# Performance work log

Hardware: AMD Instinct MI355X
Metric: run time of the kernel (lower is better)

The kernel has to match this reference:

```python
import jax, jax.numpy as jnp
import numpy as np

THRESHOLD = 6.2
N_SECTIONS = 9      # n_conv_sections
SEC_LEN = 4         # n_section_length
SEC_H = 9           # n_input_sections + n_section_length - 1
BATCH = 16384


def setup_inputs() -> dict:
    key = jax.random.key(0)
    k1, k2 = jax.random.split(key)
    # input spike-wave tensor [T, C=1, H=41, W=40]
    x = jax.random.uniform(k1, (BATCH, 1, 41, 40), dtype=jnp.float32)
    # per-section conv weights, N(0.8, 0.05) as in snn.Convolution init
    W = 0.8 + 0.05 * jax.random.normal(k2, (N_SECTIONS, 50, 1, 6, 40), dtype=jnp.float32)
    return {"x": x, "W": W}


def _conv(sec, w):
    # sec: [B,1,9,40], w: [50,1,6,40] -> [B,50,4,1]
    return jax.lax.conv_general_dilated(
        sec, w, window_strides=(1, 1), padding='VALID',
        dimension_numbers=('NCHW', 'OIHW', 'NCHW'))


def reference(x, W):
    # slice the 9 overlapping input sections -> [9, B, 1, 9, 40]
    sec = jnp.stack([x[:, :, i * SEC_LEN:i * SEC_LEN + SEC_H, :]
                     for i in range(N_SECTIONS)])
    pots = jax.vmap(_conv)(sec, W)                      # [9, B, 50, 4, 1]
    pots = jnp.max(pots, axis=3, keepdims=True)         # Pooling((4,1)) -> [9, B, 50, 1, 1]
    spks = jnp.where(pots > THRESHOLD, 1.0, 0.0).astype(pots.dtype)
    # concat sections along height (dim=2 of [B,C,H,W])
    pots_cat = jnp.moveaxis(pots[:, :, :, 0, :], 0, 2)  # [B, 50, 9, 1]
    spks_cat = jnp.moveaxis(spks[:, :, :, 0, :], 0, 2)  # [B, 50, 9, 1]
    return pots_cat, spks_cat
```

## Files before the change

### kernel.cpp

```cpp
#include <hip/hip_runtime.h>
#include <cstdint>
#include <cstddef>

#define NBATCH   16384
#define NSEC     9
#define NOC      50
#define NOCP     64
#define KREAL    240
#define KPAD     256
#define XROW     1640
#define SECELEMS 360
#define XS       392
#define OUTHALF  7372800
#define THRESH   6.2f

typedef _Float16 half8  __attribute__((ext_vector_type(8)));
typedef _Float16 half4v __attribute__((ext_vector_type(4)));
typedef float    f32x4  __attribute__((ext_vector_type(4)));

__global__ __launch_bounds__(256)
void wconv_kernel(const float* __restrict__ W, _Float16* __restrict__ wks) {
    int idx = blockIdx.x * 256 + threadIdx.x;
    int k   = idx & 255;
    int ocp = (idx >> 8) & 63;
    int sec = idx >> 14;
    float v = 0.0f;
    if (ocp < NOC && k < KREAL)
        v = W[(size_t)(sec * NOC + ocp) * KREAL + k];
    wks[idx] = (_Float16)v;
}

__global__ __launch_bounds__(256)
void conv_mfma_kernel(const float* __restrict__ x,
                      const _Float16* __restrict__ wks,
                      float* __restrict__ pots_tmp) {
    __shared__ _Float16 xs[64 * XS];

    const int tid  = threadIdx.x;
    const int tile = blockIdx.x;
    const int sec  = blockIdx.y;

    {
        half8 z = {};
        int b  = tid >> 2;
        int ko = SECELEMS + (tid & 3) * 8;
        *(half8*)&xs[b * XS + ko] = z;
    }

    const float* xg = x + (size_t)(tile * 64) * XROW + sec * 160;
    for (int c = tid; c < 64 * 90; c += 256) {
        int b  = c / 90;
        int cc = c - b * 90;
        float4 v = *(const float4*)(xg + (size_t)b * XROW + cc * 4);
        half4v h;
        h.x = (_Float16)v.x; h.y = (_Float16)v.y;
        h.z = (_Float16)v.z; h.w = (_Float16)v.w;
        *(half4v*)&xs[b * XS + cc * 4] = h;
    }
    __syncthreads();

    const int lane = tid & 63;
    const int wave = tid >> 6;
    const int l15  = lane & 15;
    const int quad = lane >> 4;

    f32x4 acc[4][4] = {};

    const _Float16* xrow = xs + (wave * 16 + l15) * XS;
    const _Float16* wrow = wks + (size_t)sec * (NOCP * KPAD) + l15 * KPAD;

    #pragma unroll
    for (int kk = 0; kk < 8; ++kk) {
        const int kb = kk * 32 + quad * 8;
        half8 av[4], bv[4];
        #pragma unroll
        for (int h = 0; h < 4; ++h)
            av[h] = *(const half8*)(xrow + h * 40 + kb);
        #pragma unroll
        for (int n = 0; n < 4; ++n)
            bv[n] = *(const half8*)(wrow + n * 16 * KPAD + kb);
        #pragma unroll
        for (int h = 0; h < 4; ++h)
            #pragma unroll
            for (int n = 0; n < 4; ++n)
                acc[h][n] = __builtin_amdgcn_mfma_f32_16x16x32_f16(
                                av[h], bv[n], acc[h][n], 0, 0, 0);
    }

    const int bbase = tile * 64 + wave * 16 + quad * 4;
    #pragma unroll
    for (int nt = 0; nt < 4; ++nt) {
        int oc = nt * 16 + l15;
        if (oc < NOC) {
            #pragma unroll
            for (int r = 0; r < 4; ++r) {
                float p = acc[0][nt][r];
                p = fmaxf(p, acc[1][nt][r]);
                p = fmaxf(p, acc[2][nt][r]);
                p = fmaxf(p, acc[3][nt][r]);
                pots_tmp[((size_t)sec * NBATCH + bbase + r) * NOC + oc] = p;
            }
        }
    }
}

__global__ __launch_bounds__(256)
void transpose_kernel(const float* __restrict__ pots_tmp,
                      float* __restrict__ out) {
    __shared__ float t[32 * 450];
    const int tid = threadIdx.x;
    const int b0  = blockIdx.x * 32;

    for (int i = tid; i < NSEC * 32 * NOC; i += 256) {
        int sec = i / (32 * NOC);
        int r   = i - sec * (32 * NOC);
        int b   = r / NOC;
        int oc  = r - b * NOC;
        float v = pots_tmp[((size_t)sec * NBATCH + b0 + b) * NOC + oc];
        t[b * 450 + oc * NSEC + sec] = v;
    }
    __syncthreads();

    float* spk = out + OUTHALF;
    for (int i = tid; i < 32 * 450; i += 256) {
        float v = t[i];
        size_t g = (size_t)b0 * 450 + i;
        out[g] = v;
        spk[g] = (v > THRESH) ? 1.0f : 0.0f;
    }
}

__global__ __launch_bounds__(256)
void naive_kernel(const float* __restrict__ x, const float* __restrict__ W,
                  float* __restrict__ out) {
    size_t idx = (size_t)blockIdx.x * 256 + threadIdx.x;
    if (idx >= OUTHALF) return;
    int s  = (int)(idx % NSEC);
    int oc = (int)((idx / NSEC) % NOC);
    int b  = (int)(idx / (NSEC * NOC));
    const float* xb = x + (size_t)b * XROW + s * 160;
    const float* w  = W + (size_t)(s * NOC + oc) * KREAL;
    float best = -1e30f;
    for (int h0 = 0; h0 < 4; ++h0) {
        float acc = 0.0f;
        for (int t = 0; t < KREAL; ++t)
            acc += xb[h0 * 40 + t] * w[t];
        best = fmaxf(best, acc);
    }
    out[idx] = best;
    out[OUTHALF + idx] = (best > THRESH) ? 1.0f : 0.0f;
}

extern "C" void kernel_launch(void* const* d_in, const int* in_sizes, int n_in,
                              void* d_out, int out_size, void* d_ws, size_t ws_size,
                              hipStream_t stream) {
    const float* x = (const float*)d_in[0];
    const float* W = (const float*)d_in[1];
    float* out = (float*)d_out;

    const size_t w_bytes   = (size_t)NSEC * NOCP * KPAD * sizeof(_Float16);
    const size_t pot_bytes = (size_t)NSEC * NBATCH * NOC * sizeof(float);

    if (ws_size < w_bytes + pot_bytes) {
        naive_kernel<<<(OUTHALF + 255) / 256, 256, 0, stream>>>(x, W, out);
        return;
    }

    _Float16* wks     = (_Float16*)d_ws;
    float*    potstmp = (float*)((char*)d_ws + w_bytes);

    wconv_kernel<<<(NSEC * NOCP * KPAD) / 256, 256, 0, stream>>>(W, wks);

    dim3 grid(NBATCH / 64, NSEC);
    conv_mfma_kernel<<<grid, 256, 0, stream>>>(x, wks, potstmp);

    transpose_kernel<<<NBATCH / 32, 256, 0, stream>>>(potstmp, out);
}
```

Measured before the change: 239.0 us.

## Fuse conv and transpose into one kernel processing all sections per batch tile

Merges the per-section MFMA conv kernel and the separate transpose kernel into one kernel. Each block loads a 16-sample batch tile once, loops over all 9 sections with each wave owning 16 output channels, and transposes the results through LDS before writing pots and spikes. This drops the pots_tmp round trip through global memory and one launch, and it reads x once instead of re-reading the overlapping section slices. The cost is a smaller MFMA tile per wave, more LDS per block (about 53 KB), and weights reloaded from global for each section.

Measured after the change: 236.7 us. No clear change (-1.0%).

```diff
diff --git a/kernel.cpp b/kernel.cpp
--- a/kernel.cpp
+++ b/kernel.cpp
@@ -9,8 +9,8 @@
 #define KREAL    240
 #define KPAD     256
 #define XROW     1640
-#define SECELEMS 360
-#define XS       392
+#define XS2      1672
+#define TB       16
 #define OUTHALF  7372800
 #define THRESH   6.2f
 
@@ -30,103 +30,85 @@
     wks[idx] = (_Float16)v;
 }
 
-__global__ __launch_bounds__(256)
-void conv_mfma_kernel(const float* __restrict__ x,
-                      const _Float16* __restrict__ wks,
-                      float* __restrict__ pots_tmp) {
-    __shared__ _Float16 xs[64 * XS];
+__global__ __launch_bounds__(256, 3)
+void fused_kernel(const float* __restrict__ x,
+                  const _Float16* __restrict__ wks,
+                  float* __restrict__ out) {
+    __shared__ __align__(16) _Float16 xs[TB * XS2];
 
-    const int tid  = threadIdx.x;
-    const int tile = blockIdx.x;
-    const int sec  = blockIdx.y;
+    const int tid = threadIdx.x;
+    const size_t b0 = (size_t)blockIdx.x * TB;
 
-    {
+    if (tid < 32) {
         half8 z = {};
-        int b  = tid >> 2;
-        int ko = SECELEMS + (tid & 3) * 8;
-        *(half8*)&xs[b * XS + ko] = z;
+        int b = tid >> 1, off = XROW + (tid & 1) * 8;
+        *(half8*)&xs[b * XS2 + off] = z;
     }
 
-    const float* xg = x + (size_t)(tile * 64) * XROW + sec * 160;
-    for (int c = tid; c < 64 * 90; c += 256) {
-        int b  = c / 90;
-        int cc = c - b * 90;
+    const float* xg = x + b0 * XROW;
+    for (int c = tid; c < TB * 410; c += 256) {
+        int b = c / 410, cc = c - b * 410;
         float4 v = *(const float4*)(xg + (size_t)b * XROW + cc * 4);
         half4v h;
         h.x = (_Float16)v.x; h.y = (_Float16)v.y;
         h.z = (_Float16)v.z; h.w = (_Float16)v.w;
-        *(half4v*)&xs[b * XS + cc * 4] = h;
+        *(half4v*)&xs[b * XS2 + cc * 4] = h;
     }
     __syncthreads();
 
     const int lane = tid & 63;
-    const int wave = tid >> 6;
+    const int w    = tid >> 6;
     const int l15  = lane & 15;
     const int quad = lane >> 4;
 
-    f32x4 acc[4][4] = {};
+    const _Float16* xrow = xs + l15 * XS2 + quad * 8;
+    const _Float16* wrow = wks + (size_t)(w * 16 + l15) * KPAD + quad * 8;
 
-    const _Float16* xrow = xs + (wave * 16 + l15) * XS;
-    const _Float16* wrow = wks + (size_t)sec * (NOCP * KPAD) + l15 * KPAD;
+    f32x4 res[NSEC];
 
-    #pragma unroll
-    for (int kk = 0; kk < 8; ++kk) {
-        const int kb = kk * 32 + quad * 8;
-        half8 av[4], bv[4];
+    for (int s = 0; s < NSEC; ++s) {
+        const _Float16* wsec = wrow + (size_t)s * (NOCP * KPAD);
+        half8 bv[8];
         #pragma unroll
-        for (int h = 0; h < 4; ++h)
-            av[h] = *(const half8*)(xrow + h * 40 + kb);
+        for (int kk = 0; kk < 8; ++kk)
+            bv[kk] = *(const half8*)(wsec + kk * 32);
+
+        f32x4 acc[4] = {f32x4{}, f32x4{}, f32x4{}, f32x4{}};
+        const _Float16* xsec = xrow + s * 160;
         #pragma unroll
-        for (int n = 0; n < 4; ++n)
-            bv[n] = *(const half8*)(wrow + n * 16 * KPAD + kb);
+        for (int kk = 0; kk < 8; ++kk) {
+            #pragma unroll
+            for (int h = 0; h < 4; ++h) {
+                half8 av = *(const half8*)(xsec + h * 40 + kk * 32);
+                acc[h] = __builtin_amdgcn_mfma_f32_16x16x32_f16(
+                             av, bv[kk], acc[h], 0, 0, 0);
+            }
+        }
+        f32x4 r;
         #pragma unroll
-        for (int h = 0; h < 4; ++h)
-            #pragma unroll
-            for (int n = 0; n < 4; ++n)
-                acc[h][n] = __builtin_amdgcn_mfma_f32_16x16x32_f16(
-                                av[h], bv[n], acc[h][n], 0, 0, 0);
+        for (int j = 0; j < 4; ++j)
+            r[j] = fmaxf(fmaxf(acc[0][j], acc[1][j]),
+                         fmaxf(acc[2][j], acc[3][j]));
+        res[s] = r;
     }
 
-    const int bbase = tile * 64 + wave * 16 + quad * 4;
-    #pragma unroll
-    for (int nt = 0; nt < 4; ++nt) {
-        int oc = nt * 16 + l15;
-        if (oc < NOC) {
+    __syncthreads();
+    float* t = (float*)xs;
+    const int oc = w * 16 + l15;
+    if (oc < NOC) {
+        #pragma unroll
+        for (int s = 0; s < NSEC; ++s)
             #pragma unroll
-            for (int r = 0; r < 4; ++r) {
-                float p = acc[0][nt][r];
-                p = fmaxf(p, acc[1][nt][r]);
-                p = fmaxf(p, acc[2][nt][r]);
-                p = fmaxf(p, acc[3][nt][r]);
-                pots_tmp[((size_t)sec * NBATCH + bbase + r) * NOC + oc] = p;
-            }
-        }
-    }
-}
-
-__global__ __launch_bounds__(256)
-void transpose_kernel(const float* __restrict__ pots_tmp,
-                      float* __restrict__ out) {
-    __shared__ float t[32 * 450];
-    const int tid = threadIdx.x;
-    const int b0  = blockIdx.x * 32;
-
-    for (int i = tid; i < NSEC * 32 * NOC; i += 256) {
-        int sec = i / (32 * NOC);
-        int r   = i - sec * (32 * NOC);
-        int b   = r / NOC;
-        int oc  = r - b * NOC;
-        float v = pots_tmp[((size_t)sec * NBATCH + b0 + b) * NOC + oc];
-        t[b * 450 + oc * NSEC + sec] = v;
+            for (int r = 0; r < 4; ++r)
+                t[(quad * 4 + r) * 450 + oc * 9 + s] = res[s][r];
     }
     __syncthreads();
 
-    float* spk = out + OUTHALF;
-    for (int i = tid; i < 32 * 450; i += 256) {
+    const size_t ob = b0 * 450;
+    for (int i = tid; i < TB * 450; i += 256) {
         float v = t[i];
-        size_t g = (size_t)b0 * 450 + i;
-        out[g] = v;
-        spk[g] = (v > THRESH) ? 1.0f : 0.0f;
+        out[ob + i] = v;
+        out[OUTHALF + ob + i] = (v > THRESH) ? 1.0f : 0.0f;
     }
 }
 
@@ -139,12 +121,12 @@
     int oc = (int)((idx / NSEC) % NOC);
     int b  = (int)(idx / (NSEC * NOC));
     const float* xb = x + (size_t)b * XROW + s * 160;
-    const float* w  = W + (size_t)(s * NOC + oc) * KREAL;
+    const float* wv = W + (size_t)(s * NOC + oc) * KREAL;
     float best = -1e30f;
     for (int h0 = 0; h0 < 4; ++h0) {
         float acc = 0.0f;
-        for (int t = 0; t < KREAL; ++t)
-            acc += xb[h0 * 40 + t] * w[t];
+        for (int k = 0; k < KREAL; ++k)
+            acc += xb[h0 * 40 + k] * wv[k];
         best = fmaxf(best, acc);
     }
     out[idx] = best;
@@ -158,21 +140,15 @@
     const float* W = (const float*)d_in[1];
     float* out = (float*)d_out;
 
-    const size_t w_bytes   = (size_t)NSEC * NOCP * KPAD * sizeof(_Float16);
-    const size_t pot_bytes = (size_t)NSEC * NBATCH * NOC * sizeof(float);
+    const size_t w_bytes = (size_t)NSEC * NOCP * KPAD * sizeof(_Float16);
 
-    if (ws_size < w_bytes + pot_bytes) {
+    if (ws_size < w_bytes) {
         naive_kernel<<<(OUTHALF + 255) / 256, 256, 0, stream>>>(x, W, out);
         return;
     }
 
-    _Float16* wks     = (_Float16*)d_ws;
-    float*    potstmp = (float*)((char*)d_ws + w_bytes);
+    _Float16* wks = (_Float16*)d_ws;
 
     wconv_kernel<<<(NSEC * NOCP * KPAD) / 256, 256, 0, stream>>>(W, wks);
-
-    dim3 grid(NBATCH / 64, NSEC);
-    conv_mfma_kernel<<<grid, 256, 0, stream>>>(x, wks, potstmp);
-
-    transpose_kernel<<<NBATCH / 32, 256, 0, stream>>>(potstmp, out);
+    fused_kernel<<<NBATCH / TB, 256, 0, stream>>>(x, wks, out);
 }
```
